# Kernel optimization log

Measured on AMD Instinct MI355X. Metric: run time of the kernel, lower is better.

## Reference

```python
import jax, jax.numpy as jnp
import numpy as np

B, T, C = 32, 4000, 128
FLOOR = 1e-12


def setup_inputs() -> dict:
    key = jax.random.key(0)
    k1, = jax.random.split(key, 1)
    x = jax.random.uniform(k1, (B, T, C), dtype=jnp.float32)  # non-negative energies
    # learned params (init values per module defaults)
    alpha = jnp.full((C,), 0.96, dtype=jnp.float32)
    delta = jnp.full((C,), 2.0, dtype=jnp.float32)
    root = jnp.full((C,), 2.0, dtype=jnp.float32)
    ema_weights = jnp.full((C,), 0.04, dtype=jnp.float32)  # per-channel smooth coef (sPCEN)
    return {"x": x, "alpha": alpha, "delta": delta, "root": root, "ema_weights": ema_weights}


def _ema(x, w):
    # x: (B,T,C), w: (C,) clamped to [0,1]; acc_t = w*x_t + (1-w)*acc_{t-1}, acc_{-1} = x_0
    w = jnp.clip(w, 0.0, 1.0).astype(x.dtype)
    init = x[:, 0, :]  # (B,C)

    def step(acc, xt):
        acc = w * xt + (1.0 - w) * acc
        return acc, acc

    _, ys = jax.lax.scan(step, init, jnp.swapaxes(x, 0, 1))  # ys: (T,B,C)
    return jnp.swapaxes(ys, 0, 1)  # (B,T,C)


def reference(x, alpha, delta, root, ema_weights):
    alpha = jnp.minimum(alpha, 1.0).astype(x.dtype)  # (C,)
    root = jnp.maximum(root, 1.0).astype(x.dtype)
    delta = delta.astype(x.dtype)
    ema = _ema(x, ema_weights)  # (B,T,C)
    one_over_root = 1.0 / root
    out = (x / (FLOOR + ema) ** alpha + delta) ** one_over_root - delta ** one_over_root
    return out
```

## Files before the change

### kernel.cpp

```cpp
#include <hip/hip_runtime.h>


#define FLOOR_EPS 1e-12f

constexpr int Bn = 32;
constexpr int Tn = 4000;
constexpr int Cn = 128;
constexpr int NCHUNK = 40;
constexpr int CHUNK  = Tn / NCHUNK;
constexpr int WARM   = 200;

__global__ __launch_bounds__(Cn) void pcen_kernel(
    const float* __restrict__ x,
    const float* __restrict__ alpha_p,
    const float* __restrict__ delta_p,
    const float* __restrict__ root_p,
    const float* __restrict__ w_p,
    float* __restrict__ out)
{
    const int c = threadIdx.x;
    const int j = blockIdx.x;
    const int b = blockIdx.y;

    const float alpha  = fminf(alpha_p[c], 1.0f);
    const float root   = fmaxf(root_p[c], 1.0f);
    const float delta  = delta_p[c];
    const float w      = fminf(fmaxf(w_p[c], 0.0f), 1.0f);
    const float omw    = 1.0f - w;
    const float oor    = 1.0f / root;
    const float droot  = __builtin_exp2f(oor * __builtin_log2f(delta));
    const float nalpha = -alpha;

    const int start = j * CHUNK;
    const int ws    = max(0, start - WARM);

    const size_t baseoff = ((size_t)b * Tn) * Cn + (size_t)c;
    const float* __restrict__ xp = x + baseoff;
    float* __restrict__ op = out + baseoff;

    float acc = xp[(size_t)ws * Cn];

    #pragma unroll 4
    for (int t = ws + 1; t < start; ++t) {
        const float xv = xp[(size_t)t * Cn];
        acc = fmaf(omw, acc, w * xv);
    }

    int t = start;
    if (j == 0) {
        const float xv = acc;
        const float l  = __builtin_log2f(FLOOR_EPS + acc);
        const float t1 = xv * __builtin_exp2f(nalpha * l);
        op[0] = __builtin_exp2f(oor * __builtin_log2f(t1 + delta)) - droot;
        t = 1;
    }

    #pragma unroll 4
    for (; t < start + CHUNK; ++t) {
        const float xv = xp[(size_t)t * Cn];
        acc = fmaf(omw, acc, w * xv);
        const float l  = __builtin_log2f(FLOOR_EPS + acc);
        const float t1 = xv * __builtin_exp2f(nalpha * l);
        op[(size_t)t * Cn] = __builtin_exp2f(oor * __builtin_log2f(t1 + delta)) - droot;
    }
}

extern "C" void kernel_launch(void* const* d_in, const int* in_sizes, int n_in,
                              void* d_out, int out_size, void* d_ws, size_t ws_size,
                              hipStream_t stream) {
    const float* x     = (const float*)d_in[0];
    const float* alpha = (const float*)d_in[1];
    const float* delta = (const float*)d_in[2];
    const float* root  = (const float*)d_in[3];
    const float* ew    = (const float*)d_in[4];
    float* out = (float*)d_out;

    dim3 grid(NCHUNK, Bn, 1);
    pcen_kernel<<<grid, Cn, 0, stream>>>(x, alpha, delta, root, ew, out);
}
```

Baseline: 159.9 us.

## Double-buffer time-step loads in registers to overlap memory latency with the scan

The per-thread time loop now loads groups of 20 time steps into two register buffers. The next group is fetched while the current one is scanned and transformed, covering both the warm-up and the output phases. The aim is to hide global-load latency in a serial, latency-bound recurrence when occupancy is low. The trade-off is higher register pressure, plus more code from fully unrolling the log/exp math per group.

```diff
diff --git a/kernel.cpp b/kernel.cpp
--- a/kernel.cpp
+++ b/kernel.cpp
@@ -9,6 +9,7 @@
 constexpr int NCHUNK = 40;
 constexpr int CHUNK  = Tn / NCHUNK;
 constexpr int WARM   = 200;
+constexpr int G      = 20;
 
 __global__ __launch_bounds__(Cn) void pcen_kernel(
     const float* __restrict__ x,
@@ -32,36 +33,54 @@
     const float nalpha = -alpha;
 
     const int start = j * CHUNK;
+    const int end   = start + CHUNK;
     const int ws    = max(0, start - WARM);
+    const int L     = end - ws;
+    const int NG    = L / G;
 
     const size_t baseoff = ((size_t)b * Tn) * Cn + (size_t)c;
     const float* __restrict__ xp = x + baseoff;
     float* __restrict__ op = out + baseoff;
+    const float* __restrict__ pl = xp + (size_t)ws * Cn;
 
-    float acc = xp[(size_t)ws * Cn];
+    float acc = pl[0];
 
-    #pragma unroll 4
-    for (int t = ws + 1; t < start; ++t) {
-        const float xv = xp[(size_t)t * Cn];
-        acc = fmaf(omw, acc, w * xv);
+    float buf0[G], buf1[G];
+
+    auto loadg = [&](float* dst, int g) {
+        const float* __restrict__ p = pl + (size_t)g * G * Cn;
+        #pragma unroll
+        for (int k = 0; k < G; ++k) dst[k] = p[(size_t)k * Cn];
+    };
+    auto compute = [&](const float* cur, int tbase) {
+        if (tbase >= start) {
+            #pragma unroll
+            for (int k = 0; k < G; ++k) {
+                const float xv = cur[k];
+                acc = fmaf(omw, acc, w * xv);
+                const float l  = __builtin_log2f(FLOOR_EPS + acc);
+                const float t1 = xv * __builtin_exp2f(nalpha * l);
+                op[(size_t)(tbase + k) * Cn] =
+                    __builtin_exp2f(oor * __builtin_log2f(t1 + delta)) - droot;
+            }
+        } else {
+            #pragma unroll
+            for (int k = 0; k < G; ++k)
+                acc = fmaf(omw, acc, w * cur[k]);
+        }
+    };
+
+    loadg(buf0, 0);
+
+    int g = 0;
+    for (; g + 1 < NG; g += 2) {
+        loadg(buf1, g + 1);
+        compute(buf0, ws + g * G);
+        if (g + 2 < NG) loadg(buf0, g + 2);
+        compute(buf1, ws + (g + 1) * G);
     }
-
-    int t = start;
-    if (j == 0) {
-        const float xv = acc;
-        const float l  = __builtin_log2f(FLOOR_EPS + acc);
-        const float t1 = xv * __builtin_exp2f(nalpha * l);
-        op[0] = __builtin_exp2f(oor * __builtin_log2f(t1 + delta)) - droot;
-        t = 1;
-    }
-
-    #pragma unroll 4
-    for (; t < start + CHUNK; ++t) {
-        const float xv = xp[(size_t)t * Cn];
-        acc = fmaf(omw, acc, w * xv);
-        const float l  = __builtin_log2f(FLOOR_EPS + acc);
-        const float t1 = xv * __builtin_exp2f(nalpha * l);
-        op[(size_t)t * Cn] = __builtin_exp2f(oor * __builtin_log2f(t1 + delta)) - droot;
+    if (g < NG) {
+        compute(buf0, ws + g * G);
     }
 }
 
```

After: 139.2 us. -12.9%, faster.

## Vectorize PCEN scan to float4 channels with double-buffered grouped prefetch

Applied to the files above, without the earlier changes.

Each thread now handles four adjacent channels through float4 loads and stores. A block of 64 threads covers two time chunks, and the chunk count doubles so each chunk is shorter. Input rows are loaded ahead in register groups of ten, double-buffered, so memory latency overlaps the serial EMA recurrence during both warm-up and output. In exchange, redundant warm-up reads per output row go up, fewer wavefronts are launched, and register use rises from the buffers.

```diff
diff --git a/kernel.cpp b/kernel.cpp
--- a/kernel.cpp
+++ b/kernel.cpp
@@ -6,11 +6,16 @@
 constexpr int Bn = 32;
 constexpr int Tn = 4000;
 constexpr int Cn = 128;
-constexpr int NCHUNK = 40;
+constexpr int NCHUNK = 80;
 constexpr int CHUNK  = Tn / NCHUNK;
 constexpr int WARM   = 200;
+constexpr int G      = 10;
+constexpr int NG     = (WARM + CHUNK) / G;
+constexpr int GW     = WARM / G;
+constexpr int ROWV   = Cn / 4;
+constexpr int CPB    = 2;
 
-__global__ __launch_bounds__(Cn) void pcen_kernel(
+__global__ __launch_bounds__(64) void pcen_kernel(
     const float* __restrict__ x,
     const float* __restrict__ alpha_p,
     const float* __restrict__ delta_p,
@@ -18,50 +23,90 @@
     const float* __restrict__ w_p,
     float* __restrict__ out)
 {
-    const int c = threadIdx.x;
-    const int j = blockIdx.x;
-    const int b = blockIdx.y;
+    const int lane = threadIdx.x & 31;
+    const int sub  = threadIdx.x >> 5;
+    const int j    = blockIdx.x * CPB + sub;
+    const int b    = blockIdx.y;
 
-    const float alpha  = fminf(alpha_p[c], 1.0f);
-    const float root   = fmaxf(root_p[c], 1.0f);
-    const float delta  = delta_p[c];
-    const float w      = fminf(fmaxf(w_p[c], 0.0f), 1.0f);
-    const float omw    = 1.0f - w;
-    const float oor    = 1.0f / root;
-    const float droot  = __builtin_exp2f(oor * __builtin_log2f(delta));
-    const float nalpha = -alpha;
+    const int c4 = lane * 4;
+    float nal[4], dl[4], oor[4], dr[4], wv[4], om[4];
+    #pragma unroll
+    for (int q = 0; q < 4; ++q) {
+        const int c = c4 + q;
+        nal[q] = -fminf(alpha_p[c], 1.0f);
+        const float root = fmaxf(root_p[c], 1.0f);
+        oor[q] = 1.0f / root;
+        dl[q]  = delta_p[c];
+        dr[q]  = __builtin_exp2f(oor[q] * __builtin_log2f(dl[q]));
+        wv[q]  = fminf(fmaxf(w_p[c], 0.0f), 1.0f);
+        om[q]  = 1.0f - wv[q];
+    }
 
     const int start = j * CHUNK;
-    const int ws    = max(0, start - WARM);
+    const int t0    = start - WARM;
 
-    const size_t baseoff = ((size_t)b * Tn) * Cn + (size_t)c;
-    const float* __restrict__ xp = x + baseoff;
-    float* __restrict__ op = out + baseoff;
+    const float4* __restrict__ xp =
+        (const float4*)(x + (size_t)b * Tn * Cn) + lane;
+    float4* __restrict__ op =
+        (float4*)(out + (size_t)b * Tn * Cn) + lane;
 
-    float acc = xp[(size_t)ws * Cn];
+    float4 buf[2][G];
+    float acc[4];
 
-    #pragma unroll 4
-    for (int t = ws + 1; t < start; ++t) {
-        const float xv = xp[(size_t)t * Cn];
-        acc = fmaf(omw, acc, w * xv);
+    auto loadg = [&](float4* dst, int g) {
+        const int tg = t0 + g * G;
+        #pragma unroll
+        for (int k = 0; k < G; ++k) {
+            int t = tg + k;
+            t = t < 0 ? 0 : t;
+            dst[k] = xp[(size_t)t * ROWV];
+        }
+    };
+    auto warmg = [&](const float4* cur) {
+        #pragma unroll
+        for (int k = 0; k < G; ++k) {
+            const float4 v = cur[k];
+            const float xv[4] = {v.x, v.y, v.z, v.w};
+            #pragma unroll
+            for (int q = 0; q < 4; ++q)
+                acc[q] = fmaf(om[q], acc[q], wv[q] * xv[q]);
+        }
+    };
+    auto emitg = [&](const float4* cur, int g) {
+        const int tg = t0 + g * G;
+        #pragma unroll
+        for (int k = 0; k < G; ++k) {
+            const float4 v = cur[k];
+            const float xv[4] = {v.x, v.y, v.z, v.w};
+            float r[4];
+            #pragma unroll
+            for (int q = 0; q < 4; ++q) {
+                acc[q] = fmaf(om[q], acc[q], wv[q] * xv[q]);
+                const float l  = __builtin_log2f(FLOOR_EPS + acc[q]);
+                const float t1 = xv[q] * __builtin_exp2f(nal[q] * l);
+                r[q] = __builtin_exp2f(oor[q] * __builtin_log2f(t1 + dl[q])) - dr[q];
+            }
+            op[(size_t)(tg + k) * ROWV] = make_float4(r[0], r[1], r[2], r[3]);
+        }
+    };
+
+    loadg(buf[0], 0);
+    {
+        const float4 v0 = buf[0][0];
+        acc[0] = v0.x; acc[1] = v0.y; acc[2] = v0.z; acc[3] = v0.w;
     }
 
-    int t = start;
-    if (j == 0) {
-        const float xv = acc;
-        const float l  = __builtin_log2f(FLOOR_EPS + acc);
-        const float t1 = xv * __builtin_exp2f(nalpha * l);
-        op[0] = __builtin_exp2f(oor * __builtin_log2f(t1 + delta)) - droot;
-        t = 1;
+    for (int g = 0; g < GW; g += 2) {
+        loadg(buf[1], g + 1);
+        warmg(buf[0]);
+        loadg(buf[0], g + 2);
+        warmg(buf[1]);
     }
 
-    #pragma unroll 4
-    for (; t < start + CHUNK; ++t) {
-        const float xv = xp[(size_t)t * Cn];
-        acc = fmaf(omw, acc, w * xv);
-        const float l  = __builtin_log2f(FLOOR_EPS + acc);
-        const float t1 = xv * __builtin_exp2f(nalpha * l);
-        op[(size_t)t * Cn] = __builtin_exp2f(oor * __builtin_log2f(t1 + delta)) - droot;
+    #pragma unroll
+    for (int e = GW; e < NG; ++e) {
+        if (e + 1 < NG) loadg(buf[(e + 1) & 1], e + 1);
+        emitg(buf[e & 1], e);
     }
 }
 
@@ -75,6 +120,6 @@
     const float* ew    = (const float*)d_in[4];
     float* out = (float*)d_out;
 
-    dim3 grid(NCHUNK, Bn, 1);
-    pcen_kernel<<<grid, Cn, 0, stream>>>(x, alpha, delta, root, ew, out);
+    dim3 grid(NCHUNK / CPB, Bn, 1);
+    pcen_kernel<<<grid, 64, 0, stream>>>(x, alpha, delta, root, ew, out);
 }
```

After: 159.7 us. Within noise of the previous version (-0.2%).
